# Optimization experiments

Hardware: AMD Instinct MI355X
Metric: run time of the kernel (lower is better)

Reference implementation:

```python
import jax, jax.numpy as jnp
import numpy as np

H, D, C, K, N, B = 16, 64, 1024, 256, 4096, 2

def setup_inputs() -> dict:
    key = jax.random.key(0)
    ks = jax.random.split(key, 10)
    s = lambda k, shp, fan: jax.random.normal(k, shp, jnp.float32) * (1.0 / np.sqrt(fan))
    return {
        "x": jax.random.normal(ks[0], (B, N, C), jnp.float32),
        "Wq": s(ks[1], (H, D, C), C),   # per-head Linear(channels->dim), no bias
        "Wk": s(ks[2], (H, D, C), C),
        "Wv": s(ks[3], (H, D, C), C),
        "We": s(ks[4], (H, K, N), N),   # E: Linear(input_size->dim_k)
        "bE": jnp.zeros((H, K), jnp.float32),
        "Wf": s(ks[5], (H, K, N), N),   # F: Linear(input_size->dim_k)
        "bF": jnp.zeros((H, K), jnp.float32),
        "Wo": s(ks[6], (C, H * D), H * D),
        "bo": jnp.zeros((C,), jnp.float32),
    }

def reference(x, Wq, Wk, Wv, We, bE, Wf, bF, Wo, bo):
    b, n, c = x.shape
    h, d = Wq.shape[0], Wq.shape[1]
    # per-head Q/K/V projections, vectorized over heads: [b,h,n,d]
    Q = jnp.einsum('bnc,hdc->bhnd', x, Wq)
    Kt = jnp.einsum('bnc,hdc->bhdn', x, Wk)   # K already transposed(1,2)
    Vt = jnp.einsum('bnc,hdc->bhdn', x, Wv)   # V transposed(1,2)
    # Linformer E/F low-rank projections along sequence axis -> [b,h,d,k]
    Ke = jnp.einsum('bhdn,hkn->bhdk', Kt, We) + bE[None, :, None, :]
    Vf = jnp.einsum('bhdn,hkn->bhdk', Vt, Wf) + bF[None, :, None, :]
    # scaled scores + softmax over low-rank dim k
    scores = jnp.einsum('bhnd,bhdk->bhnk', Q, Kt if False else Ke) / jnp.sqrt(jnp.asarray(d, x.dtype))
    P = jax.nn.softmax(scores, axis=-1)
    # P @ V_f^T  -> [b,h,n,d]
    out = jnp.einsum('bhnk,bhkd->bhnd', P, jnp.swapaxes(Vf, -1, -2))
    # concat heads -> [b,n,h*d]
    out = jnp.transpose(out, (0, 2, 1, 3)).reshape(b, n, h * d)
    out = jax.nn.gelu(out, approximate=False)
    return out @ Wo.T + bo
```

## Files before the change

### kernel.cpp

```cpp
#include <hip/hip_runtime.h>

typedef unsigned short u16;
typedef float f32x4 __attribute__((ext_vector_type(4)));
typedef short s16x8 __attribute__((ext_vector_type(8)));
typedef unsigned short u16x4 __attribute__((ext_vector_type(4)));

__device__ __forceinline__ u16 f2bf(float f) {
  union { float f; unsigned u; } v; v.f = f;
  unsigned r = v.u + 0x7FFFu + ((v.u >> 16) & 1u);
  return (u16)(r >> 16);
}

__device__ __forceinline__ void gload_lds16(const void* g, void* l) {
  __builtin_amdgcn_global_load_lds(
      (const __attribute__((address_space(1))) void*)g,
      (__attribute__((address_space(3))) void*)l, 16, 0, 0);
}

__global__ __launch_bounds__(256) void cast_f32_bf16(
    const float* __restrict__ src, u16* __restrict__ dst, int n4) {
  int i = blockIdx.x * 256 + threadIdx.x;
  if (i >= n4) return;
  f32x4 v = ((const f32x4*)src)[i];
  u16x4 o = { f2bf(v[0]), f2bf(v[1]), f2bf(v[2]), f2bf(v[3]) };
  ((u16x4*)dst)[i] = o;
}

template <int FINAL>
__global__ __launch_bounds__(256, 2) void gemm_pipe(
    const u16* __restrict__ A, const u16* __restrict__ B,
    void* __restrict__ Cout, const float* __restrict__ bias,
    int K, int lda, int ldb, int ldc) {
  __shared__ char smem[3 * 8192 + 3 * 16384];
  const int tid = threadIdx.x;
  const int wid = tid >> 6, lane = tid & 63;
  const int lo = lane & 15, hi = lane >> 4;
  const int wr = wid >> 1, wc = wid & 1;
  const long brow = (long)blockIdx.y * 128;
  const long bcol = (long)blockIdx.x * 256;
  const int T = K >> 5;

  f32x4 acc[4][8] = {};

  const char* Ab = (const char*)(A + (size_t)brow * lda);
  const char* Bb = (const char*)(B + (size_t)bcol * ldb);
  const size_t ldab = (size_t)lda * 2, ldbb = (size_t)ldb * 2;

  const int LA0 = wid * 2048 + lane * 16, LA1 = LA0 + 1024;
  const int LB0 = wid * 4096 + lane * 16, LB1 = LB0 + 1024;
  const int LB2 = LB0 + 2048, LB3 = LB0 + 3072;
#define SRCCOL(L) (((L) & 63) ^ ((((L) >> 7) & 3) << 4))
  const char* aS0 = Ab + (size_t)(LA0 >> 6) * ldab + SRCCOL(LA0);
  const char* aS1 = Ab + (size_t)(LA1 >> 6) * ldab + SRCCOL(LA1);
  const char* bS0 = Bb + (size_t)(LB0 >> 6) * ldbb + SRCCOL(LB0);
  const char* bS1 = Bb + (size_t)(LB1 >> 6) * ldbb + SRCCOL(LB1);
  const char* bS2 = Bb + (size_t)(LB2 >> 6) * ldbb + SRCCOL(LB2);
  const char* bS3 = Bb + (size_t)(LB3 >> 6) * ldbb + SRCCOL(LB3);
#undef SRCCOL

  int ra[4], rb[8];
#pragma unroll
  for (int m = 0; m < 4; ++m) {
    int row = wr * 64 + m * 16 + lo;
    ra[m] = row * 64 + ((hi ^ ((row >> 1) & 3)) << 4);
  }
#pragma unroll
  for (int n = 0; n < 8; ++n) {
    int row = wc * 128 + n * 16 + lo;
    rb[n] = row * 64 + ((hi ^ ((row >> 1) & 3)) << 4);
  }

#define STAGE(t)                                                    \
  {                                                                 \
    char* sa_ = smem + ((t) % 3) * 8192;                            \
    char* sb_ = smem + 24576 + ((t) % 3) * 16384;                   \
    size_t kb_ = (size_t)(t) << 6;                                  \
    gload_lds16(aS0 + kb_, sa_ + LA0);                              \
    gload_lds16(aS1 + kb_, sa_ + LA1);                              \
    gload_lds16(bS0 + kb_, sb_ + LB0);                              \
    gload_lds16(bS1 + kb_, sb_ + LB1);                              \
    gload_lds16(bS2 + kb_, sb_ + LB2);                              \
    gload_lds16(bS3 + kb_, sb_ + LB3);                              \
  }

  STAGE(0); STAGE(1);
  asm volatile("s_waitcnt vmcnt(6)" ::: "memory");
  __builtin_amdgcn_s_barrier();
  __builtin_amdgcn_sched_barrier(0);

  for (int t = 0; t < T; ++t) {
    const char* sa = smem + (t % 3) * 8192;
    const char* sb = smem + 24576 + (t % 3) * 16384;
    s16x8 af[4], bf[8];
#pragma unroll
    for (int m = 0; m < 4; ++m) af[m] = *(const s16x8*)(sa + ra[m]);
#pragma unroll
    for (int n = 0; n < 8; ++n) bf[n] = *(const s16x8*)(sb + rb[n]);
    if (t + 2 < T) STAGE(t + 2);
    __builtin_amdgcn_s_setprio(1);
#pragma unroll
    for (int m = 0; m < 4; ++m)
#pragma unroll
      for (int n = 0; n < 8; ++n)
        acc[m][n] = __builtin_amdgcn_mfma_f32_16x16x32_bf16(af[m], bf[n], acc[m][n], 0, 0, 0);
    __builtin_amdgcn_s_setprio(0);
    if (t + 2 < T) asm volatile("s_waitcnt vmcnt(6)" ::: "memory");
    else           asm volatile("s_waitcnt vmcnt(0)" ::: "memory");
    __builtin_amdgcn_s_barrier();
    __builtin_amdgcn_sched_barrier(0);
  }
#undef STAGE

#pragma unroll
  for (int m = 0; m < 4; ++m) {
#pragma unroll
    for (int n = 0; n < 8; ++n) {
#pragma unroll
      for (int r = 0; r < 4; ++r) {
        size_t row = brow + wr * 64 + m * 16 + hi * 4 + r;
        size_t col = bcol + wc * 128 + n * 16 + lo;
        float v = acc[m][n][r];
        if (FINAL) ((float*)Cout)[row * ldc + col] = v + bias[col];
        else       ((u16*)Cout)[row * ldc + col] = f2bf(v);
      }
    }
  }
}

__global__ __launch_bounds__(256) void kevf_kernel(
    const float* __restrict__ We, const float* __restrict__ Wf,
    const u16* __restrict__ QKV, float* __restrict__ part) {
  __shared__ u16 Vt[2][64 * 64];
  const int type = blockIdx.z >> 2, ns = blockIdx.z & 3;
  const int bh = blockIdx.y, b = bh >> 4, h = bh & 15;
  const int kk0 = blockIdx.x * 64;
  const float* W = (type ? Wf : We) + ((size_t)(h * 256 + kk0)) * 4096;
  const int col0 = (type ? 2048 : 1024) + h * 64;
  const int tid = threadIdx.x, wid = tid >> 6, lane = tid & 63;
  const int lo = lane & 15, hi = lane >> 4;
  const int nbeg = ns << 10;

  const int rr = wid * 16 + lo;
  const float* wsrc = W + (size_t)rr * 4096 + nbeg + hi * 8;
  const int qn = tid >> 2, qc = (tid & 3) * 16;
  const u16* qsrc = QKV + ((size_t)b * 4096 + nbeg + qn) * 3072 + col0 + qc;

  f32x4 acc[4] = {};
  f32x4 w[3][4];
  s16x8 q[3][2];

#define KISSUE(t) {                                       \
    const float* wp_ = wsrc + (size_t)(t) * 64;           \
    w[(t) % 3][0] = *(const f32x4*)wp_;                   \
    w[(t) % 3][1] = *(const f32x4*)(wp_ + 4);             \
    w[(t) % 3][2] = *(const f32x4*)(wp_ + 32);            \
    w[(t) % 3][3] = *(const f32x4*)(wp_ + 36);            \
    const u16* qp_ = qsrc + (size_t)(t) * 64 * 3072;      \
    q[(t) % 3][0] = *(const s16x8*)qp_;                   \
    q[(t) % 3][1] = *(const s16x8*)(qp_ + 8); }

  KISSUE(0); KISSUE(1); KISSUE(2);
#pragma unroll
  for (int t = 0; t < 16; ++t) {
    u16* vb = Vt[t & 1];
#pragma unroll
    for (int e = 0; e < 16; ++e) {
      int dd = qc + e;
      int sw = (dd & 7) ^ ((dd >> 4) & 3);
      u16 val = (e < 8) ? (u16)q[t % 3][0][e] : (u16)q[t % 3][1][e - 8];
      vb[dd * 64 + (qn ^ (sw << 3))] = val;
    }
    s16x8 a0, a1;
#pragma unroll
    for (int j = 0; j < 4; ++j) {
      a0[j]     = (short)f2bf(w[t % 3][0][j]);
      a0[j + 4] = (short)f2bf(w[t % 3][1][j]);
      a1[j]     = (short)f2bf(w[t % 3][2][j]);
      a1[j + 4] = (short)f2bf(w[t % 3][3][j]);
    }
    if (t + 3 < 16) KISSUE(t + 3);
    __syncthreads();
#pragma unroll
    for (int dt = 0; dt < 4; ++dt) {
      int dd = dt * 16 + lo;
      int sw = (lo & 7) ^ dt;
      s16x8 b0 = *(const s16x8*)&vb[dd * 64 + ((hi * 8) ^ (sw << 3))];
      s16x8 b1 = *(const s16x8*)&vb[dd * 64 + ((32 + hi * 8) ^ (sw << 3))];
      acc[dt] = __builtin_amdgcn_mfma_f32_16x16x32_bf16(a0, b0, acc[dt], 0, 0, 0);
      acc[dt] = __builtin_amdgcn_mfma_f32_16x16x32_bf16(a1, b1, acc[dt], 0, 0, 0);
    }
  }
#undef KISSUE

  const size_t pbase = ((size_t)((type * 32 + bh) * 4 + blockIdx.x) * 4 + ns) * 4096;
#pragma unroll
  for (int dt = 0; dt < 4; ++dt)
#pragma unroll
    for (int rg = 0; rg < 4; ++rg) {
      int kkl = wid * 16 + hi * 4 + rg;
      int dd = dt * 16 + lo;
      part[pbase + kkl * 64 + dd] = acc[dt][rg];
    }
}

__global__ __launch_bounds__(256) void kevf_reduce(
    const float* __restrict__ part, const float* __restrict__ bE,
    const float* __restrict__ bF, u16* __restrict__ KeT, u16* __restrict__ Vf) {
  const int tb = blockIdx.x;
  const int type = tb >> 7, bh = (tb >> 2) & 31, kc = tb & 3;
  const int t = threadIdx.x;
  const int kkl = t >> 2, dd0 = (t & 3) * 16;
  const float* p = part + (size_t)tb * 16384 + kkl * 64 + dd0;
  f32x4 s[4];
#pragma unroll
  for (int j = 0; j < 4; ++j) s[j] = ((const f32x4*)p)[j];
#pragma unroll
  for (int ns = 1; ns < 4; ++ns)
#pragma unroll
    for (int j = 0; j < 4; ++j) {
      f32x4 v = ((const f32x4*)(p + ns * 4096))[j];
      s[j][0] += v[0]; s[j][1] += v[1]; s[j][2] += v[2]; s[j][3] += v[3];
    }
  const int kk = kc * 64 + kkl;
  const float bias = (type ? bF : bE)[(bh & 15) * 256 + kk];
  if (type == 0) {
    u16* o = KeT + ((size_t)bh * 256 + kk) * 64 + dd0;
#pragma unroll
    for (int j = 0; j < 4; ++j) {
      u16x4 w = { f2bf(s[j][0] + bias), f2bf(s[j][1] + bias),
                  f2bf(s[j][2] + bias), f2bf(s[j][3] + bias) };
      *(u16x4*)(o + j * 4) = w;
    }
  } else {
#pragma unroll
    for (int j = 0; j < 4; ++j)
#pragma unroll
      for (int e = 0; e < 4; ++e) {
        int dd = dd0 + j * 4 + e;
        Vf[((size_t)bh * 64 + dd) * 256 + kk] = f2bf(s[j][e] + bias);
      }
  }
}

__global__ __launch_bounds__(256) void attn_fused(
    const u16* __restrict__ QKV, const u16* __restrict__ KeT,
    const u16* __restrict__ Vf, u16* __restrict__ attn) {
  __shared__ char smem[65536];
  char* sKe = smem;
  char* sVf = smem + 32768;
  const int tid = threadIdx.x, wid = tid >> 6, lane = tid & 63;
  const int lo = lane & 15, hi = lane >> 4;
  const int bh = blockIdx.y, b = bh >> 4, h = bh & 15;
  const int n0 = blockIdx.x * 64;

  const char* keg = (const char*)(KeT + (size_t)bh * 256 * 64);
  const char* vfg = (const char*)(Vf + (size_t)bh * 64 * 256);
#pragma unroll
  for (int i = 0; i < 8; ++i) {
    int ob = wid * 8192 + i * 1024;
    int o = ob + lane * 16;
    int kr = o >> 7, kc = o & 127;
    gload_lds16(keg + kr * 128 + (kc ^ ((kr & 7) << 4)), sKe + ob);
    int vr = o >> 9, vc = o & 511;
    gload_lds16(vfg + vr * 512 + (vc ^ ((vr & 7) << 4)), sVf + ob);
  }
  const u16* qp = QKV + (size_t)(b * 4096 + n0 + wid * 16 + lo) * 3072 + h * 64;
  s16x8 qf0 = *(const s16x8*)(qp + hi * 8);
  s16x8 qf1 = *(const s16x8*)(qp + 32 + hi * 8);
  __syncthreads();

  f32x4 sc[16];
#pragma unroll
  for (int nt = 0; nt < 16; ++nt) {
    int kk = nt * 16 + lo;
    int sw = (kk & 7) << 4;
    s16x8 b0 = *(const s16x8*)(sKe + kk * 128 + ((hi * 16) ^ sw));
    s16x8 b1 = *(const s16x8*)(sKe + kk * 128 + ((64 + hi * 16) ^ sw));
    f32x4 c = {0.f, 0.f, 0.f, 0.f};
    c = __builtin_amdgcn_mfma_f32_16x16x32_bf16(qf0, b0, c, 0, 0, 0);
    c = __builtin_amdgcn_mfma_f32_16x16x32_bf16(qf1, b1, c, 0, 0, 0);
    sc[nt] = c;
  }
  float mx[4], inv[4];
#pragma unroll
  for (int r = 0; r < 4; ++r) {
    float m = sc[0][r];
#pragma unroll
    for (int nt = 1; nt < 16; ++nt) m = fmaxf(m, sc[nt][r]);
    m = fmaxf(m, __shfl_xor(m, 1));
    m = fmaxf(m, __shfl_xor(m, 2));
    m = fmaxf(m, __shfl_xor(m, 4));
    m = fmaxf(m, __shfl_xor(m, 8));
    mx[r] = m;
  }
  const float SCL = 0.125f * 1.4426950408889634f;
  float sm[4] = {0.f, 0.f, 0.f, 0.f};
#pragma unroll
  for (int nt = 0; nt < 16; ++nt)
#pragma unroll
    for (int r = 0; r < 4; ++r) {
      float p = exp2f((sc[nt][r] - mx[r]) * SCL);
      sc[nt][r] = p;
      sm[r] += p;
    }
#pragma unroll
  for (int r = 0; r < 4; ++r) {
    float s = sm[r];
    s += __shfl_xor(s, 1);
    s += __shfl_xor(s, 2);
    s += __shfl_xor(s, 4);
    s += __shfl_xor(s, 8);
    inv[r] = 1.0f / s;
  }
  __syncthreads();
  char* pb = smem + wid * 8192;
#pragma unroll
  for (int nt = 0; nt < 16; ++nt)
#pragma unroll
    for (int r = 0; r < 4; ++r) {
      int row = hi * 4 + r;
      int kk = nt * 16 + lo;
      *(u16*)(pb + row * 512 + ((kk * 2) ^ ((row & 7) << 4))) = f2bf(sc[nt][r] * inv[r]);
    }
  __syncthreads();
  s16x8 pa[8];
#pragma unroll
  for (int ks = 0; ks < 8; ++ks)
    pa[ks] = *(const s16x8*)(pb + lo * 512 + ((ks * 64 + hi * 16) ^ ((lo & 7) << 4)));
#pragma unroll
  for (int dt = 0; dt < 4; ++dt) {
    int dd = dt * 16 + lo;
    int sw = (dd & 7) << 4;
    f32x4 o = {0.f, 0.f, 0.f, 0.f};
#pragma unroll
    for (int ks = 0; ks < 8; ++ks) {
      s16x8 vb = *(const s16x8*)(sVf + dd * 512 + ((ks * 64 + hi * 16) ^ sw));
      o = __builtin_amdgcn_mfma_f32_16x16x32_bf16(pa[ks], vb, o, 0, 0, 0);
    }
#pragma unroll
    for (int r = 0; r < 4; ++r) {
      int row = n0 + wid * 16 + hi * 4 + r;
      float x = o[r];
      float g = 0.5f * x * (1.0f + erff(x * 0.7071067811865476f));
      attn[(size_t)(b * 4096 + row) * 1024 + h * 64 + dd] = f2bf(g);
    }
  }
}

extern "C" void kernel_launch(void* const* d_in, const int* in_sizes, int n_in,
                              void* d_out, int out_size, void* d_ws, size_t ws_size,
                              hipStream_t stream) {
  const float* x  = (const float*)d_in[0];
  const float* Wq = (const float*)d_in[1];
  const float* Wk = (const float*)d_in[2];
  const float* Wv = (const float*)d_in[3];
  const float* We = (const float*)d_in[4];
  const float* bE = (const float*)d_in[5];
  const float* Wf = (const float*)d_in[6];
  const float* bF = (const float*)d_in[7];
  const float* Wo = (const float*)d_in[8];
  const float* bo = (const float*)d_in[9];
  float* out = (float*)d_out;

  char* ws = (char*)d_ws;
  u16* xb   = (u16*)(ws);
  u16* Wqkv = (u16*)(ws + 16777216);
  u16* Wob  = (u16*)(ws + 23068672);
  u16* QKV  = (u16*)(ws + 25165824);
  u16* KeT  = (u16*)(ws + 75497472);
  u16* Vf   = (u16*)(ws + 76546048);
  u16* attn = (u16*)(ws + 77594624);
  float* part = (float*)(ws);

  cast_f32_bf16<<<8192, 256, 0, stream>>>(x, xb, 2097152);
  cast_f32_bf16<<<1024, 256, 0, stream>>>(Wq, Wqkv, 262144);
  cast_f32_bf16<<<1024, 256, 0, stream>>>(Wk, Wqkv + 1048576, 262144);
  cast_f32_bf16<<<1024, 256, 0, stream>>>(Wv, Wqkv + 2097152, 262144);
  cast_f32_bf16<<<1024, 256, 0, stream>>>(Wo, Wob, 262144);

  gemm_pipe<0><<<dim3(12, 64), 256, 0, stream>>>(xb, Wqkv, QKV, nullptr,
                                                 1024, 1024, 1024, 3072);
  kevf_kernel<<<dim3(4, 32, 8), 256, 0, stream>>>(We, Wf, QKV, part);
  kevf_reduce<<<256, 256, 0, stream>>>(part, bE, bF, KeT, Vf);
  attn_fused<<<dim3(64, 32), 256, 0, stream>>>(QKV, KeT, Vf, attn);
  gemm_pipe<1><<<dim3(4, 64), 256, 0, stream>>>(attn, Wob, out, bo,
                                                1024, 1024, 1024, 1024);
}
```

Before: 200.6 us.

## Emit K and V transposed from QKV GEMM and pipeline kevf through LDS

The QKV GEMM epilogue now writes Q row-major and K/V in a per-head transposed [b,h,d,n] layout, so the low-rank E/F projection kernel can stream K/V tiles straight into LDS with async global-to-LDS loads. Previously it gathered strided QKV elements and scattered them element by element into a transposed LDS tile. The kevf kernel is reworked into a double/triple-buffered pipeline with explicit waitcnt and barriers. Because the operand roles are swapped, the partial sums come out in a different orientation, and the reduce kernel's output mapping changes to match. The cost is strided 8-byte transposed stores in the GEMM epilogue and more LDS use per block.

```diff
diff --git a/kernel.cpp b/kernel.cpp
--- a/kernel.cpp
+++ b/kernel.cpp
@@ -26,10 +26,11 @@
   ((u16x4*)dst)[i] = o;
 }
 
-template <int FINAL>
+template <int MODE>
 __global__ __launch_bounds__(256, 2) void gemm_pipe(
     const u16* __restrict__ A, const u16* __restrict__ B,
     void* __restrict__ Cout, const float* __restrict__ bias,
+    u16* __restrict__ KT, u16* __restrict__ VT,
     int K, int lda, int ldb, int ldc) {
   __shared__ char smem[3 * 8192 + 3 * 16384];
   const int tid = threadIdx.x;
@@ -111,96 +112,145 @@
   }
 #undef STAGE
 
-#pragma unroll
-  for (int m = 0; m < 4; ++m) {
-#pragma unroll
-    for (int n = 0; n < 8; ++n) {
-#pragma unroll
-      for (int r = 0; r < 4; ++r) {
-        size_t row = brow + wr * 64 + m * 16 + hi * 4 + r;
-        size_t col = bcol + wc * 128 + n * 16 + lo;
-        float v = acc[m][n][r];
-        if (FINAL) ((float*)Cout)[row * ldc + col] = v + bias[col];
-        else       ((u16*)Cout)[row * ldc + col] = f2bf(v);
-      }
+  if (MODE == 1) {
+#pragma unroll
+    for (int m = 0; m < 4; ++m)
+#pragma unroll
+      for (int n = 0; n < 8; ++n)
+#pragma unroll
+        for (int r = 0; r < 4; ++r) {
+          size_t row = brow + wr * 64 + m * 16 + hi * 4 + r;
+          size_t col = bcol + wc * 128 + n * 16 + lo;
+          ((float*)Cout)[row * ldc + col] = acc[m][n][r] + bias[col];
+        }
+  } else {
+    const int kind = (int)(bcol >> 10);
+    if (kind == 0) {
+#pragma unroll
+      for (int m = 0; m < 4; ++m)
+#pragma unroll
+        for (int n = 0; n < 8; ++n)
+#pragma unroll
+          for (int r = 0; r < 4; ++r) {
+            size_t row = brow + wr * 64 + m * 16 + hi * 4 + r;
+            size_t col = bcol + wc * 128 + n * 16 + lo;
+            ((u16*)Cout)[row * 1024 + col] = f2bf(acc[m][n][r]);
+          }
+    } else {
+      u16* Tp = (kind == 1) ? KT : VT;
+#pragma unroll
+      for (int m = 0; m < 4; ++m)
+#pragma unroll
+        for (int n = 0; n < 8; ++n) {
+          int col = (int)(bcol + wc * 128 + n * 16 + lo);
+          int lc = col & 1023, h = lc >> 6, d = lc & 63;
+          size_t n0 = brow + wr * 64 + m * 16 + hi * 4;
+          int b = (int)(n0 >> 12), nin = (int)(n0 & 4095);
+          u16x4 w = { f2bf(acc[m][n][0]), f2bf(acc[m][n][1]),
+                      f2bf(acc[m][n][2]), f2bf(acc[m][n][3]) };
+          *(u16x4*)(Tp + (((size_t)b * 16 + h) * 64 + d) * 4096 + nin) = w;
+        }
     }
   }
 }
 
 __global__ __launch_bounds__(256) void kevf_kernel(
     const float* __restrict__ We, const float* __restrict__ Wf,
-    const u16* __restrict__ QKV, float* __restrict__ part) {
-  __shared__ u16 Vt[2][64 * 64];
+    const u16* __restrict__ KT, const u16* __restrict__ VT,
+    float* __restrict__ part) {
+  __shared__ u16 As[2][64 * 64];
+  __shared__ u16 Bs[3][64 * 64];
   const int type = blockIdx.z >> 2, ns = blockIdx.z & 3;
-  const int bh = blockIdx.y, b = bh >> 4, h = bh & 15;
+  const int bh = blockIdx.y, h = bh & 15;
   const int kk0 = blockIdx.x * 64;
   const float* W = (type ? Wf : We) + ((size_t)(h * 256 + kk0)) * 4096;
-  const int col0 = (type ? 2048 : 1024) + h * 64;
+  const u16* T = (type ? VT : KT) + (size_t)bh * 64 * 4096;
   const int tid = threadIdx.x, wid = tid >> 6, lane = tid & 63;
   const int lo = lane & 15, hi = lane >> 4;
   const int nbeg = ns << 10;
 
-  const int rr = wid * 16 + lo;
-  const float* wsrc = W + (size_t)rr * 4096 + nbeg + hi * 8;
-  const int qn = tid >> 2, qc = (tid & 3) * 16;
-  const u16* qsrc = QKV + ((size_t)b * 4096 + nbeg + qn) * 3072 + col0 + qc;
+  const int wrow = tid >> 2;
+  const float* wsrc = W + (size_t)wrow * 4096 + nbeg + (tid & 3) * 16;
+  const int aw0 = wrow * 128 + (((tid & 3) * 32) ^ ((wrow & 7) << 4));
+  const int aw1 = wrow * 128 + (((tid & 3) * 32 + 16) ^ ((wrow & 7) << 4));
+  const int L0 = tid * 16, L1 = 4096 + tid * 16;
+  const int tr0 = L0 >> 7, tc0 = (L0 & 127) ^ ((tr0 & 7) << 4);
+  const int tr1 = L1 >> 7, tc1 = (L1 & 127) ^ ((tr1 & 7) << 4);
+  const char* tS0 = (const char*)(T + (size_t)tr0 * 4096 + nbeg) + tc0;
+  const char* tS1 = (const char*)(T + (size_t)tr1 * 4096 + nbeg) + tc1;
+
+  const int dd = wid * 16 + lo;
+  const int raK0 = dd * 128 + ((hi * 16) ^ ((dd & 7) << 4));
+  const int raK1 = dd * 128 + ((64 + hi * 16) ^ ((dd & 7) << 4));
+  int rbW[4][2];
+#pragma unroll
+  for (int dt = 0; dt < 4; ++dt) {
+    int r = dt * 16 + lo;
+    rbW[dt][0] = r * 128 + ((hi * 16) ^ ((r & 7) << 4));
+    rbW[dt][1] = r * 128 + ((64 + hi * 16) ^ ((r & 7) << 4));
+  }
 
   f32x4 acc[4] = {};
-  f32x4 w[3][4];
-  s16x8 q[3][2];
-
-#define KISSUE(t) {                                       \
-    const float* wp_ = wsrc + (size_t)(t) * 64;           \
-    w[(t) % 3][0] = *(const f32x4*)wp_;                   \
-    w[(t) % 3][1] = *(const f32x4*)(wp_ + 4);             \
-    w[(t) % 3][2] = *(const f32x4*)(wp_ + 32);            \
-    w[(t) % 3][3] = *(const f32x4*)(wp_ + 36);            \
-    const u16* qp_ = qsrc + (size_t)(t) * 64 * 3072;      \
-    q[(t) % 3][0] = *(const s16x8*)qp_;                   \
-    q[(t) % 3][1] = *(const s16x8*)(qp_ + 8); }
-
-  KISSUE(0); KISSUE(1); KISSUE(2);
-#pragma unroll
-  for (int t = 0; t < 16; ++t) {
-    u16* vb = Vt[t & 1];
-#pragma unroll
-    for (int e = 0; e < 16; ++e) {
-      int dd = qc + e;
-      int sw = (dd & 7) ^ ((dd >> 4) & 3);
-      u16 val = (e < 8) ? (u16)q[t % 3][0][e] : (u16)q[t % 3][1][e - 8];
-      vb[dd * 64 + (qn ^ (sw << 3))] = val;
-    }
-    s16x8 a0, a1;
-#pragma unroll
-    for (int j = 0; j < 4; ++j) {
-      a0[j]     = (short)f2bf(w[t % 3][0][j]);
-      a0[j + 4] = (short)f2bf(w[t % 3][1][j]);
-      a1[j]     = (short)f2bf(w[t % 3][2][j]);
-      a1[j + 4] = (short)f2bf(w[t % 3][3][j]);
-    }
-    if (t + 3 < 16) KISSUE(t + 3);
-    __syncthreads();
-#pragma unroll
-    for (int dt = 0; dt < 4; ++dt) {
-      int dd = dt * 16 + lo;
-      int sw = (lo & 7) ^ dt;
-      s16x8 b0 = *(const s16x8*)&vb[dd * 64 + ((hi * 8) ^ (sw << 3))];
-      s16x8 b1 = *(const s16x8*)&vb[dd * 64 + ((32 + hi * 8) ^ (sw << 3))];
-      acc[dt] = __builtin_amdgcn_mfma_f32_16x16x32_bf16(a0, b0, acc[dt], 0, 0, 0);
-      acc[dt] = __builtin_amdgcn_mfma_f32_16x16x32_bf16(a1, b1, acc[dt], 0, 0, 0);
-    }
-  }
-#undef KISSUE
+  f32x4 Aw0, Aw1, Aw2, Aw3, Bw0, Bw1, Bw2, Bw3;
+
+#define WISSUE(S, t) { const float* p_ = wsrc + (size_t)(t) * 64;  \
+    S##w0 = *(const f32x4*)p_;       S##w1 = *(const f32x4*)(p_ + 4); \
+    S##w2 = *(const f32x4*)(p_ + 8); S##w3 = *(const f32x4*)(p_ + 12); }
+#define TISSUE(t) { size_t kb_ = (size_t)(t) * 128;                \
+    gload_lds16(tS0 + kb_, (char*)Bs[(t) % 3] + L0);               \
+    gload_lds16(tS1 + kb_, (char*)Bs[(t) % 3] + L1); }
+
+#define KSTEP(S, t) {                                                     \
+    if ((t) < 14) asm volatile("s_waitcnt vmcnt(6)" ::: "memory");        \
+    else          asm volatile("s_waitcnt vmcnt(0)" ::: "memory");        \
+    s16x8 w0_, w1_;                                                       \
+    _Pragma("unroll")                                                     \
+    for (int j = 0; j < 4; ++j) {                                         \
+      w0_[j]     = (short)f2bf(S##w0[j]); w0_[j + 4] = (short)f2bf(S##w1[j]); \
+      w1_[j]     = (short)f2bf(S##w2[j]); w1_[j + 4] = (short)f2bf(S##w3[j]); \
+    }                                                                     \
+    *(s16x8*)((char*)As[(t) & 1] + aw0) = w0_;                            \
+    *(s16x8*)((char*)As[(t) & 1] + aw1) = w1_;                            \
+    asm volatile("s_waitcnt lgkmcnt(0)" ::: "memory");                    \
+    __builtin_amdgcn_s_barrier();                                         \
+    __builtin_amdgcn_sched_barrier(0);                                    \
+    const char* bs_ = (const char*)Bs[(t) % 3];                           \
+    const char* as_ = (const char*)As[(t) & 1];                           \
+    s16x8 a0_ = *(const s16x8*)(bs_ + raK0);                              \
+    s16x8 a1_ = *(const s16x8*)(bs_ + raK1);                              \
+    s16x8 bfr_[4][2];                                                     \
+    _Pragma("unroll")                                                     \
+    for (int dt = 0; dt < 4; ++dt) {                                      \
+      bfr_[dt][0] = *(const s16x8*)(as_ + rbW[dt][0]);                    \
+      bfr_[dt][1] = *(const s16x8*)(as_ + rbW[dt][1]);                    \
+    }                                                                     \
+    if ((t) + 2 < 16) { WISSUE(S, (t) + 2); TISSUE((t) + 2); }            \
+    __builtin_amdgcn_s_setprio(1);                                        \
+    _Pragma("unroll")                                                     \
+    for (int dt = 0; dt < 4; ++dt) {                                      \
+      acc[dt] = __builtin_amdgcn_mfma_f32_16x16x32_bf16(a0_, bfr_[dt][0], acc[dt], 0, 0, 0); \
+      acc[dt] = __builtin_amdgcn_mfma_f32_16x16x32_bf16(a1_, bfr_[dt][1], acc[dt], 0, 0, 0); \
+    }                                                                     \
+    __builtin_amdgcn_s_setprio(0);                                        \
+    __builtin_amdgcn_s_barrier();                                         \
+    __builtin_amdgcn_sched_barrier(0);                                    \
+  }
+
+  WISSUE(A, 0); TISSUE(0); WISSUE(B, 1); TISSUE(1);
+  KSTEP(A, 0);  KSTEP(B, 1);  KSTEP(A, 2);  KSTEP(B, 3);
+  KSTEP(A, 4);  KSTEP(B, 5);  KSTEP(A, 6);  KSTEP(B, 7);
+  KSTEP(A, 8);  KSTEP(B, 9);  KSTEP(A, 10); KSTEP(B, 11);
+  KSTEP(A, 12); KSTEP(B, 13); KSTEP(A, 14); KSTEP(B, 15);
+#undef WISSUE
+#undef TISSUE
+#undef KSTEP
 
   const size_t pbase = ((size_t)((type * 32 + bh) * 4 + blockIdx.x) * 4 + ns) * 4096;
 #pragma unroll
   for (int dt = 0; dt < 4; ++dt)
 #pragma unroll
-    for (int rg = 0; rg < 4; ++rg) {
-      int kkl = wid * 16 + hi * 4 + rg;
-      int dd = dt * 16 + lo;
-      part[pbase + kkl * 64 + dd] = acc[dt][rg];
-    }
+    for (int r = 0; r < 4; ++r)
+      part[pbase + (size_t)(wid * 16 + hi * 4 + r) * 64 + dt * 16 + lo] = acc[dt][r];
 }
 
 __global__ __launch_bounds__(256) void kevf_reduce(
@@ -209,8 +259,8 @@
   const int tb = blockIdx.x;
   const int type = tb >> 7, bh = (tb >> 2) & 31, kc = tb & 3;
   const int t = threadIdx.x;
-  const int kkl = t >> 2, dd0 = (t & 3) * 16;
-  const float* p = part + (size_t)tb * 16384 + kkl * 64 + dd0;
+  const int dd = t >> 2, kkc = (t & 3) * 16;
+  const float* p = part + (size_t)tb * 16384 + dd * 64 + kkc;
   f32x4 s[4];
 #pragma unroll
   for (int j = 0; j < 4; ++j) s[j] = ((const f32x4*)p)[j];
@@ -221,29 +271,29 @@
       f32x4 v = ((const f32x4*)(p + ns * 4096))[j];
       s[j][0] += v[0]; s[j][1] += v[1]; s[j][2] += v[2]; s[j][3] += v[3];
     }
-  const int kk = kc * 64 + kkl;
-  const float bias = (type ? bF : bE)[(bh & 15) * 256 + kk];
+  const int h = bh & 15;
+  const float* bv = (type ? bF : bE) + h * 256 + kc * 64 + kkc;
   if (type == 0) {
-    u16* o = KeT + ((size_t)bh * 256 + kk) * 64 + dd0;
+#pragma unroll
+    for (int j = 0; j < 4; ++j)
+#pragma unroll
+      for (int e = 0; e < 4; ++e) {
+        int kk = kkc + j * 4 + e;
+        KeT[((size_t)bh * 256 + kc * 64 + kk) * 64 + dd] = f2bf(s[j][e] + bv[j * 4 + e]);
+      }
+  } else {
+    u16* o = Vf + ((size_t)bh * 64 + dd) * 256 + kc * 64 + kkc;
 #pragma unroll
     for (int j = 0; j < 4; ++j) {
-      u16x4 w = { f2bf(s[j][0] + bias), f2bf(s[j][1] + bias),
-                  f2bf(s[j][2] + bias), f2bf(s[j][3] + bias) };
+      u16x4 w = { f2bf(s[j][0] + bv[j * 4 + 0]), f2bf(s[j][1] + bv[j * 4 + 1]),
+                  f2bf(s[j][2] + bv[j * 4 + 2]), f2bf(s[j][3] + bv[j * 4 + 3]) };
       *(u16x4*)(o + j * 4) = w;
     }
-  } else {
-#pragma unroll
-    for (int j = 0; j < 4; ++j)
-#pragma unroll
-      for (int e = 0; e < 4; ++e) {
-        int dd = dd0 + j * 4 + e;
-        Vf[((size_t)bh * 64 + dd) * 256 + kk] = f2bf(s[j][e] + bias);
-      }
   }
 }
 
 __global__ __launch_bounds__(256) void attn_fused(
-    const u16* __restrict__ QKV, const u16* __restrict__ KeT,
+    const u16* __restrict__ Q, const u16* __restrict__ KeT,
     const u16* __restrict__ Vf, u16* __restrict__ attn) {
   __shared__ char smem[65536];
   char* sKe = smem;
@@ -264,7 +314,7 @@
     int vr = o >> 9, vc = o & 511;
     gload_lds16(vfg + vr * 512 + (vc ^ ((vr & 7) << 4)), sVf + ob);
   }
-  const u16* qp = QKV + (size_t)(b * 4096 + n0 + wid * 16 + lo) * 3072 + h * 64;
+  const u16* qp = Q + (size_t)(b * 4096 + n0 + wid * 16 + lo) * 1024 + h * 64;
   s16x8 qf0 = *(const s16x8*)(qp + hi * 8);
   s16x8 qf1 = *(const s16x8*)(qp + 32 + hi * 8);
   __syncthreads();
@@ -366,7 +416,9 @@
   u16* xb   = (u16*)(ws);
   u16* Wqkv = (u16*)(ws + 16777216);
   u16* Wob  = (u16*)(ws + 23068672);
-  u16* QKV  = (u16*)(ws + 25165824);
+  u16* Q    = (u16*)(ws + 25165824);
+  u16* KT   = (u16*)(ws + 41943040);
+  u16* VT   = (u16*)(ws + 58720256);
   u16* KeT  = (u16*)(ws + 75497472);
   u16* Vf   = (u16*)(ws + 76546048);
   u16* attn = (u16*)(ws + 77594624);
@@ -378,11 +430,11 @@
   cast_f32_bf16<<<1024, 256, 0, stream>>>(Wv, Wqkv + 2097152, 262144);
   cast_f32_bf16<<<1024, 256, 0, stream>>>(Wo, Wob, 262144);
 
-  gemm_pipe<0><<<dim3(12, 64), 256, 0, stream>>>(xb, Wqkv, QKV, nullptr,
-                                                 1024, 1024, 1024, 3072);
-  kevf_kernel<<<dim3(4, 32, 8), 256, 0, stream>>>(We, Wf, QKV, part);
+  gemm_pipe<0><<<dim3(12, 64), 256, 0, stream>>>(xb, Wqkv, Q, nullptr, KT, VT,
+                                                 1024, 1024, 1024, 1024);
+  kevf_kernel<<<dim3(4, 32, 8), 256, 0, stream>>>(We, Wf, KT, VT, part);
   kevf_reduce<<<256, 256, 0, stream>>>(part, bE, bF, KeT, Vf);
-  attn_fused<<<dim3(64, 32), 256, 0, stream>>>(QKV, KeT, Vf, attn);
-  gemm_pipe<1><<<dim3(4, 64), 256, 0, stream>>>(attn, Wob, out, bo,
+  attn_fused<<<dim3(64, 32), 256, 0, stream>>>(Q, KeT, Vf, attn);
+  gemm_pipe<1><<<dim3(4, 64), 256, 0, stream>>>(attn, Wob, out, bo, nullptr, nullptr,
                                                 1024, 1024, 1024, 1024);
 }
```

Result: no change. 201.2 us (+0.3%).
